# Kernel optimization log

Hardware: AMD Instinct MI355X
Metric: run time of the kernel (lower is better)

Reference implementation:

```python
import jax, jax.numpy as jnp
import numpy as np

# LIF decay constants: alpha = exp(-dt/tau_syn), beta = exp(-dt/tau_mem)
ALPHA = float(np.exp(-0.001 / 0.01))   # ~0.9048
BETA = float(np.exp(-0.001 / 0.005))   # ~0.8187


@jax.custom_vjp
def spike_fn(x):
    # HeavisideSigmoidApprox: Heaviside forward, sigmoid-derivative surrogate backward
    return (x > 0).astype(x.dtype)

def _spike_fwd(x):
    return spike_fn(x), x

def _spike_bwd(x, g):
    s = jax.nn.sigmoid(x)
    return (g * s * (1.0 - s),)

spike_fn.defvjp(_spike_fwd, _spike_bwd)


def lif_layer(spikes_in, W, R):
    """spikes_in: [B,T,F] -> (spikes [B,T,H], potentials [B,T,H])"""
    h = jnp.einsum('btf,fo->bto', spikes_in, W)  # [B,T,H]
    B, T, H = h.shape
    zeros = jnp.zeros((B, H), h.dtype)

    def step(carry, h_t):
        cur, pot, spk = carry
        rec = spk @ R                      # recurrent current from previous spikes
        new_spk = spike_fn(pot - 1.0)      # threshold at 1.0
        active = 1.0 - jax.lax.stop_gradient(new_spk)  # reset: .detach() in torch
        new_cur = ALPHA * cur + h_t + rec
        new_pot = (BETA * pot + new_cur) * active
        return (new_cur, new_pot, new_spk), (new_pot, new_spk)

    _, (pots, spks) = jax.lax.scan(step, (zeros, zeros, zeros), jnp.swapaxes(h, 0, 1))
    return jnp.swapaxes(spks, 0, 1), jnp.swapaxes(pots, 0, 1)


def readout_rnn(spikes, Wout):
    """spikes: [B,T,H] -> output potentials [B,T+1,O] (leading zero record)"""
    h = jnp.einsum('btf,fo->bto', spikes, Wout)  # [B,T,O]
    B, T, O = h.shape
    zeros = jnp.zeros((B, O), h.dtype)

    def step(carry, h_t):
        cur, pot = carry
        cur = ALPHA * cur + h_t
        pot = BETA * pot + cur
        return (cur, pot), pot

    _, pots = jax.lax.scan(step, (zeros, zeros), jnp.swapaxes(h, 0, 1))
    return jnp.concatenate([zeros[:, None, :], jnp.swapaxes(pots, 0, 1)], axis=1)


def _xavier(key, shape):
    std = np.sqrt(2.0 / (shape[0] + shape[1]))
    return jax.random.normal(key, shape, dtype=jnp.float32) * std


def setup_inputs() -> dict:
    key = jax.random.key(0)
    ks = jax.random.split(key, 6)
    B, T, F, H, O = 256, 100, 256, 1024, 8
    return {
        'inputs': jax.random.normal(ks[0], (B, T, F), dtype=jnp.float32),
        'W0': _xavier(ks[1], (F, H)),
        'W1': _xavier(ks[2], (H, H)),
        'R0': _xavier(ks[3], (H, H)),
        'R1': _xavier(ks[4], (H, H)),
        'Wout': _xavier(ks[5], (H, O)),
    }


def reference(inputs, W0, W1, R0, R1, Wout):
    s1, v1 = lif_layer(inputs, W0, R0)
    s2, v2 = lif_layer(s1, W1, R1)
    out = readout_rnn(s2, Wout)  # [B, T+1, O]
    return (out, s1, s2, v1, v2)
```

## Files before the change

### kernel.cpp

```cpp
#include <hip/hip_runtime.h>


#define SNN_B 256
#define SNN_T 100
#define SNN_F 256
#define SNN_H 1024
#define SNN_O 8

#define ALPHA 0.9048374180359595f
#define BETA  0.8187307530779818f

__global__ __launch_bounds__(256) void gemm_f32(
    const float* __restrict__ A, const float* __restrict__ Bm,
    float* __restrict__ C, int M, int N, int K)
{
    __shared__ float As[2][8][132];
    __shared__ float Bs[2][8][132];

    const int tid = threadIdx.x;
    const int m0 = blockIdx.y * 128;
    const int n0 = blockIdx.x * 128;
    const int ty = tid >> 4;
    const int tx = tid & 15;

    const int arow = tid >> 1;
    const int akq  = (tid & 1) * 4;
    const int bkr  = tid >> 5;
    const int bnq  = (tid & 31) * 4;

    const float* Aptr = A + (size_t)(m0 + arow) * K + akq;
    const float* Bptr = Bm + (size_t)bkr * N + n0 + bnq;

    float4 ar = *(const float4*)Aptr;
    float4 br = *(const float4*)Bptr;
    As[0][akq + 0][arow] = ar.x;
    As[0][akq + 1][arow] = ar.y;
    As[0][akq + 2][arow] = ar.z;
    As[0][akq + 3][arow] = ar.w;
    *(float4*)&Bs[0][bkr][bnq] = br;
    __syncthreads();

    float acc[8][8] = {};
    const int NK = K >> 3;

    for (int kt = 0; kt < NK; ++kt) {
        const int cur = kt & 1;
        if (kt + 1 < NK) {
            ar = *(const float4*)(Aptr + (kt + 1) * 8);
            br = *(const float4*)(Bptr + (size_t)(kt + 1) * 8 * N);
        }
        #pragma unroll
        for (int k = 0; k < 8; ++k) {
            const float4 a0 = *(const float4*)&As[cur][k][ty * 8];
            const float4 a1 = *(const float4*)&As[cur][k][ty * 8 + 4];
            const float4 b0 = *(const float4*)&Bs[cur][k][tx * 8];
            const float4 b1 = *(const float4*)&Bs[cur][k][tx * 8 + 4];
            const float am[8] = {a0.x, a0.y, a0.z, a0.w, a1.x, a1.y, a1.z, a1.w};
            const float bn[8] = {b0.x, b0.y, b0.z, b0.w, b1.x, b1.y, b1.z, b1.w};
            #pragma unroll
            for (int i = 0; i < 8; ++i)
                #pragma unroll
                for (int j = 0; j < 8; ++j)
                    acc[i][j] = fmaf(am[i], bn[j], acc[i][j]);
        }
        if (kt + 1 < NK) {
            const int nxt = cur ^ 1;
            __syncthreads();
            As[nxt][akq + 0][arow] = ar.x;
            As[nxt][akq + 1][arow] = ar.y;
            As[nxt][akq + 2][arow] = ar.z;
            As[nxt][akq + 3][arow] = ar.w;
            *(float4*)&Bs[nxt][bkr][bnq] = br;
            __syncthreads();
        }
    }

    #pragma unroll
    for (int i = 0; i < 8; ++i) {
        float* crow = C + (size_t)(m0 + ty * 8 + i) * N + n0 + tx * 8;
        *(float4*)crow = make_float4(acc[i][0], acc[i][1], acc[i][2], acc[i][3]);
        *(float4*)(crow + 4) = make_float4(acc[i][4], acc[i][5], acc[i][6], acc[i][7]);
    }
}


#define LIF_LOAD(Xa, Xb, Xc, Xd, Xe, Xf, Xg, Xh, cidx)                        \
    {                                                                         \
        const int4 ka_ = *(const int4*)&slist[(cidx) << 3];                   \
        const int4 kb_ = *(const int4*)&slist[(((cidx) << 3) + 4)];           \
        Xa = R[((unsigned)ka_.x << 10) | ctid];                               \
        Xb = R[((unsigned)ka_.y << 10) | ctid];                               \
        Xc = R[((unsigned)ka_.z << 10) | ctid];                               \
        Xd = R[((unsigned)ka_.w << 10) | ctid];                               \
        Xe = R[((unsigned)kb_.x << 10) | ctid];                               \
        Xf = R[((unsigned)kb_.y << 10) | ctid];                               \
        Xg = R[((unsigned)kb_.z << 10) | ctid];                               \
        Xh = R[((unsigned)kb_.w << 10) | ctid];                               \
    }

#define LIF_SUM(Xa, Xb, Xc, Xd, Xe, Xf, Xg, Xh)                               \
    {                                                                         \
        a0 += Xa; a0 += Xb; a0 += Xc; a0 += Xd;                               \
        a0 += Xe; a0 += Xf; a0 += Xg; a0 += Xh;                               \
    }

__global__ __launch_bounds__(1024) void lif_scan(
    const float* __restrict__ hbuf,
    const float* __restrict__ R,
    float* __restrict__ s_out,
    float* __restrict__ v_out)
{
    __shared__ __align__(16) int slist[SNN_H];
    __shared__ int wtot[16];
    __shared__ int sn;

    const int tid = threadIdx.x;
    const unsigned ctid = (unsigned)tid;
    const int b = blockIdx.x;
    const int wv = tid >> 6;
    const int lane = tid & 63;

    float cur = 0.f, pot = 0.f;

    if (tid == 0) sn = 0;
    __syncthreads();

    const float* hrow = hbuf + (size_t)b * SNN_T * SNN_H + tid;
    float*       srow = s_out + (size_t)b * SNN_T * SNN_H + tid;
    float*       vrow = v_out + (size_t)b * SNN_T * SNN_H + tid;

    for (int t = 0; t < SNN_T; ++t) {
        const float hv = *hrow;
        hrow += SNN_H;

        const int n = sn;
        float a0 = 0.f;
        int i = 0;
        const int nc = n >> 3;
        if (nc > 0) {
            float A0, A1, A2, A3, A4, A5, A6, A7;
            float B0, B1, B2, B3, B4, B5, B6, B7;
            LIF_LOAD(A0, A1, A2, A3, A4, A5, A6, A7, 0);
            int c = 1;
            for (; c + 1 < nc; c += 2) {
                LIF_LOAD(B0, B1, B2, B3, B4, B5, B6, B7, c);
                LIF_SUM(A0, A1, A2, A3, A4, A5, A6, A7);
                LIF_LOAD(A0, A1, A2, A3, A4, A5, A6, A7, c + 1);
                LIF_SUM(B0, B1, B2, B3, B4, B5, B6, B7);
            }
            if (c < nc) {
                LIF_LOAD(B0, B1, B2, B3, B4, B5, B6, B7, c);
                LIF_SUM(A0, A1, A2, A3, A4, A5, A6, A7);
                LIF_SUM(B0, B1, B2, B3, B4, B5, B6, B7);
            } else {
                LIF_SUM(A0, A1, A2, A3, A4, A5, A6, A7);
            }
            i = nc << 3;
        }
        for (; i < n; ++i)
            a0 += R[((unsigned)slist[i] << 10) | ctid];

        const bool p = (pot - 1.0f) > 0.0f;
        const float s = p ? 1.0f : 0.0f;
        cur = fmaf(ALPHA, cur, hv) + a0;
        pot = fmaf(BETA, pot, cur) * (1.0f - s);

        *srow = s;
        *vrow = pot;
        srow += SNN_H; vrow += SNN_H;

        const unsigned long long m = __ballot(p);
        const unsigned long long lt = (1ull << lane) - 1ull;
        const int lpre = __popcll(m & lt);
        if (lane == 0) wtot[wv] = __popcll(m);
        __syncthreads();
        int off = lpre;
        #pragma unroll
        for (int q = 0; q < 15; ++q)
            if (q < wv) off += wtot[q];
        if (p) slist[off] = tid;
        if (tid == 0) {
            int stot = 0;
            #pragma unroll
            for (int q = 0; q < 16; ++q) stot += wtot[q];
            sn = stot;
        }
        __syncthreads();
    }
}

__global__ __launch_bounds__(256) void readout_gemm(
    const float* __restrict__ s2in, const float* __restrict__ Wout,
    float* __restrict__ h3)
{
    const int gid = blockIdx.x * 256 + threadIdx.x;
    const int row = gid >> 3;
    const int o = gid & 7;
    const float* srow = s2in + (size_t)row * SNN_H;
    float acc = 0.f;
    for (int k = 0; k < SNN_H; k += 4) {
        float4 s = *(const float4*)&srow[k];
        acc = fmaf(s.x, Wout[(k + 0) * SNN_O + o], acc);
        acc = fmaf(s.y, Wout[(k + 1) * SNN_O + o], acc);
        acc = fmaf(s.z, Wout[(k + 2) * SNN_O + o], acc);
        acc = fmaf(s.w, Wout[(k + 3) * SNN_O + o], acc);
    }
    h3[(size_t)row * SNN_O + o] = acc;
}

__global__ __launch_bounds__(256) void readout_scan(
    const float* __restrict__ h3, float* __restrict__ out)
{
    const int gid = blockIdx.x * 256 + threadIdx.x;
    const int b = gid >> 3;
    const int o = gid & 7;
    float c = 0.f, p = 0.f;
    out[((size_t)b * (SNN_T + 1) + 0) * SNN_O + o] = 0.f;
    for (int t = 0; t < SNN_T; ++t) {
        c = fmaf(ALPHA, c, h3[((size_t)b * SNN_T + t) * SNN_O + o]);
        p = fmaf(BETA, p, c);
        out[((size_t)b * (SNN_T + 1) + t + 1) * SNN_O + o] = p;
    }
}

extern "C" void kernel_launch(void* const* d_in, const int* in_sizes, int n_in,
                              void* d_out, int out_size, void* d_ws, size_t ws_size,
                              hipStream_t stream)
{
    const float* X    = (const float*)d_in[0];
    const float* W0   = (const float*)d_in[1];
    const float* W1   = (const float*)d_in[2];
    const float* R0   = (const float*)d_in[3];
    const float* R1   = (const float*)d_in[4];
    const float* Wout = (const float*)d_in[5];

    const size_t BT_H = (size_t)SNN_B * SNN_T * SNN_H;
    float* out = (float*)d_out;
    float* s1  = out + (size_t)SNN_B * (SNN_T + 1) * SNN_O;
    float* s2  = s1 + BT_H;
    float* v1  = s2 + BT_H;
    float* v2  = v1 + BT_H;

    float* ws   = (float*)d_ws;
    float* hbuf = ws;
    float* h3   = hbuf + BT_H;

    const int M = SNN_B * SNN_T;

    gemm_f32<<<dim3(SNN_H / 128, M / 128), 256, 0, stream>>>(X, W0, hbuf, M, SNN_H, SNN_F);

    lif_scan<<<SNN_B, 1024, 0, stream>>>(hbuf, R0, s1, v1);

    gemm_f32<<<dim3(SNN_H / 128, M / 128), 256, 0, stream>>>(s1, W1, hbuf, M, SNN_H, SNN_H);

    lif_scan<<<SNN_B, 1024, 0, stream>>>(hbuf, R1, s2, v2);

    readout_gemm<<<(M * SNN_O) / 256, 256, 0, stream>>>(s2, Wout, h3);
    readout_scan<<<(SNN_B * SNN_O) / 256, 256, 0, stream>>>(h3, out);
}
```

Before: 3.108 ms.

## Deepen GEMM K-tile, pre-shift spike indices, restructure readout GEMM per row

The main GEMM now stages 16 K values per shared-memory tile instead of 8, which halves the number of barrier pairs per tile loop at the cost of more shared memory. The LIF scan stores spike indices already shifted to byte offsets, so each recurrent gather becomes a single OR plus byte-pointer load with no shift. The readout GEMM now has one thread per row that computes all 8 outputs, reading each spike row once instead of eight times and writing float4 results. The trade-off is fewer threads in the readout kernel.

New measurement: 3.393 ms. +9.2%, slower.

```diff
diff --git a/kernel.cpp b/kernel.cpp
--- a/kernel.cpp
+++ b/kernel.cpp
@@ -14,8 +14,8 @@
     const float* __restrict__ A, const float* __restrict__ Bm,
     float* __restrict__ C, int M, int N, int K)
 {
-    __shared__ float As[2][8][132];
-    __shared__ float Bs[2][8][132];
+    __shared__ float As[2][16][132];
+    __shared__ float Bs[2][16][132];
 
     const int tid = threadIdx.x;
     const int m0 = blockIdx.y * 128;
@@ -24,39 +24,50 @@
     const int tx = tid & 15;
 
     const int arow = tid >> 1;
-    const int akq  = (tid & 1) * 4;
-    const int bkr  = tid >> 5;
+    const int ak0  = (tid & 1) * 4;
+    const int bk0  = tid >> 5;
     const int bnq  = (tid & 31) * 4;
 
-    const float* Aptr = A + (size_t)(m0 + arow) * K + akq;
-    const float* Bptr = Bm + (size_t)bkr * N + n0 + bnq;
-
-    float4 ar = *(const float4*)Aptr;
-    float4 br = *(const float4*)Bptr;
-    As[0][akq + 0][arow] = ar.x;
-    As[0][akq + 1][arow] = ar.y;
-    As[0][akq + 2][arow] = ar.z;
-    As[0][akq + 3][arow] = ar.w;
-    *(float4*)&Bs[0][bkr][bnq] = br;
+    const float* Aptr = A + (size_t)(m0 + arow) * K;
+    const float* Bptr = Bm + n0 + bnq;
+
+    float4 a0r = *(const float4*)(Aptr + ak0);
+    float4 a1r = *(const float4*)(Aptr + ak0 + 8);
+    float4 b0r = *(const float4*)(Bptr + (size_t)bk0 * N);
+    float4 b1r = *(const float4*)(Bptr + (size_t)(bk0 + 8) * N);
+    As[0][ak0 + 0][arow] = a0r.x;
+    As[0][ak0 + 1][arow] = a0r.y;
+    As[0][ak0 + 2][arow] = a0r.z;
+    As[0][ak0 + 3][arow] = a0r.w;
+    As[0][ak0 + 8][arow] = a1r.x;
+    As[0][ak0 + 9][arow] = a1r.y;
+    As[0][ak0 + 10][arow] = a1r.z;
+    As[0][ak0 + 11][arow] = a1r.w;
+    *(float4*)&Bs[0][bk0][bnq] = b0r;
+    *(float4*)&Bs[0][bk0 + 8][bnq] = b1r;
     __syncthreads();
 
     float acc[8][8] = {};
-    const int NK = K >> 3;
+    const int NK = K >> 4;
 
     for (int kt = 0; kt < NK; ++kt) {
         const int cur = kt & 1;
         if (kt + 1 < NK) {
-            ar = *(const float4*)(Aptr + (kt + 1) * 8);
-            br = *(const float4*)(Bptr + (size_t)(kt + 1) * 8 * N);
+            const float* Ap = Aptr + (kt + 1) * 16;
+            const float* Bp = Bptr + (size_t)(kt + 1) * 16 * N;
+            a0r = *(const float4*)(Ap + ak0);
+            a1r = *(const float4*)(Ap + ak0 + 8);
+            b0r = *(const float4*)(Bp + (size_t)bk0 * N);
+            b1r = *(const float4*)(Bp + (size_t)(bk0 + 8) * N);
         }
         #pragma unroll
-        for (int k = 0; k < 8; ++k) {
-            const float4 a0 = *(const float4*)&As[cur][k][ty * 8];
-            const float4 a1 = *(const float4*)&As[cur][k][ty * 8 + 4];
-            const float4 b0 = *(const float4*)&Bs[cur][k][tx * 8];
-            const float4 b1 = *(const float4*)&Bs[cur][k][tx * 8 + 4];
-            const float am[8] = {a0.x, a0.y, a0.z, a0.w, a1.x, a1.y, a1.z, a1.w};
-            const float bn[8] = {b0.x, b0.y, b0.z, b0.w, b1.x, b1.y, b1.z, b1.w};
+        for (int k = 0; k < 16; ++k) {
+            const float4 av0 = *(const float4*)&As[cur][k][ty * 8];
+            const float4 av1 = *(const float4*)&As[cur][k][ty * 8 + 4];
+            const float4 bv0 = *(const float4*)&Bs[cur][k][tx * 8];
+            const float4 bv1 = *(const float4*)&Bs[cur][k][tx * 8 + 4];
+            const float am[8] = {av0.x, av0.y, av0.z, av0.w, av1.x, av1.y, av1.z, av1.w};
+            const float bn[8] = {bv0.x, bv0.y, bv0.z, bv0.w, bv1.x, bv1.y, bv1.z, bv1.w};
             #pragma unroll
             for (int i = 0; i < 8; ++i)
                 #pragma unroll
@@ -66,11 +77,16 @@
         if (kt + 1 < NK) {
             const int nxt = cur ^ 1;
             __syncthreads();
-            As[nxt][akq + 0][arow] = ar.x;
-            As[nxt][akq + 1][arow] = ar.y;
-            As[nxt][akq + 2][arow] = ar.z;
-            As[nxt][akq + 3][arow] = ar.w;
-            *(float4*)&Bs[nxt][bkr][bnq] = br;
+            As[nxt][ak0 + 0][arow] = a0r.x;
+            As[nxt][ak0 + 1][arow] = a0r.y;
+            As[nxt][ak0 + 2][arow] = a0r.z;
+            As[nxt][ak0 + 3][arow] = a0r.w;
+            As[nxt][ak0 + 8][arow] = a1r.x;
+            As[nxt][ak0 + 9][arow] = a1r.y;
+            As[nxt][ak0 + 10][arow] = a1r.z;
+            As[nxt][ak0 + 11][arow] = a1r.w;
+            *(float4*)&Bs[nxt][bk0][bnq] = b0r;
+            *(float4*)&Bs[nxt][bk0 + 8][bnq] = b1r;
             __syncthreads();
         }
     }
@@ -88,14 +104,14 @@
     {                                                                         \
         const int4 ka_ = *(const int4*)&slist[(cidx) << 3];                   \
         const int4 kb_ = *(const int4*)&slist[(((cidx) << 3) + 4)];           \
-        Xa = R[((unsigned)ka_.x << 10) | ctid];                               \
-        Xb = R[((unsigned)ka_.y << 10) | ctid];                               \
-        Xc = R[((unsigned)ka_.z << 10) | ctid];                               \
-        Xd = R[((unsigned)ka_.w << 10) | ctid];                               \
-        Xe = R[((unsigned)kb_.x << 10) | ctid];                               \
-        Xf = R[((unsigned)kb_.y << 10) | ctid];                               \
-        Xg = R[((unsigned)kb_.z << 10) | ctid];                               \
-        Xh = R[((unsigned)kb_.w << 10) | ctid];                               \
+        Xa = *(const float*)(Rb + (unsigned)(ka_.x | tid4));                  \
+        Xb = *(const float*)(Rb + (unsigned)(ka_.y | tid4));                  \
+        Xc = *(const float*)(Rb + (unsigned)(ka_.z | tid4));                  \
+        Xd = *(const float*)(Rb + (unsigned)(ka_.w | tid4));                  \
+        Xe = *(const float*)(Rb + (unsigned)(kb_.x | tid4));                  \
+        Xf = *(const float*)(Rb + (unsigned)(kb_.y | tid4));                  \
+        Xg = *(const float*)(Rb + (unsigned)(kb_.z | tid4));                  \
+        Xh = *(const float*)(Rb + (unsigned)(kb_.w | tid4));                  \
     }
 
 #define LIF_SUM(Xa, Xb, Xc, Xd, Xe, Xf, Xg, Xh)                               \
@@ -115,10 +131,11 @@
     __shared__ int sn;
 
     const int tid = threadIdx.x;
-    const unsigned ctid = (unsigned)tid;
+    const int tid4 = tid << 2;
     const int b = blockIdx.x;
     const int wv = tid >> 6;
     const int lane = tid & 63;
+    const char* __restrict__ Rb = (const char*)R;
 
     float cur = 0.f, pot = 0.f;
 
@@ -158,7 +175,7 @@
             i = nc << 3;
         }
         for (; i < n; ++i)
-            a0 += R[((unsigned)slist[i] << 10) | ctid];
+            a0 += *(const float*)(Rb + (unsigned)(slist[i] | tid4));
 
         const bool p = (pot - 1.0f) > 0.0f;
         const float s = p ? 1.0f : 0.0f;
@@ -178,7 +195,7 @@
         #pragma unroll
         for (int q = 0; q < 15; ++q)
             if (q < wv) off += wtot[q];
-        if (p) slist[off] = tid;
+        if (p) slist[off] = tid << 12;
         if (tid == 0) {
             int stot = 0;
             #pragma unroll
@@ -193,19 +210,21 @@
     const float* __restrict__ s2in, const float* __restrict__ Wout,
     float* __restrict__ h3)
 {
-    const int gid = blockIdx.x * 256 + threadIdx.x;
-    const int row = gid >> 3;
-    const int o = gid & 7;
+    const int row = blockIdx.x * 256 + threadIdx.x;
     const float* srow = s2in + (size_t)row * SNN_H;
-    float acc = 0.f;
+    float acc[8] = {};
     for (int k = 0; k < SNN_H; k += 4) {
-        float4 s = *(const float4*)&srow[k];
-        acc = fmaf(s.x, Wout[(k + 0) * SNN_O + o], acc);
-        acc = fmaf(s.y, Wout[(k + 1) * SNN_O + o], acc);
-        acc = fmaf(s.z, Wout[(k + 2) * SNN_O + o], acc);
-        acc = fmaf(s.w, Wout[(k + 3) * SNN_O + o], acc);
-    }
-    h3[(size_t)row * SNN_O + o] = acc;
+        const float4 s = *(const float4*)&srow[k];
+        const float sv[4] = {s.x, s.y, s.z, s.w};
+        #pragma unroll
+        for (int kk = 0; kk < 4; ++kk)
+            #pragma unroll
+            for (int o = 0; o < 8; ++o)
+                acc[o] = fmaf(sv[kk], Wout[(size_t)(k + kk) * SNN_O + o], acc[o]);
+    }
+    float* hp = h3 + (size_t)row * SNN_O;
+    *(float4*)hp = make_float4(acc[0], acc[1], acc[2], acc[3]);
+    *(float4*)(hp + 4) = make_float4(acc[4], acc[5], acc[6], acc[7]);
 }
 
 __global__ __launch_bounds__(256) void readout_scan(
@@ -255,6 +274,6 @@
 
     lif_scan<<<SNN_B, 1024, 0, stream>>>(hbuf, R1, s2, v2);
 
-    readout_gemm<<<(M * SNN_O) / 256, 256, 0, stream>>>(s2, Wout, h3);
+    readout_gemm<<<M / 256, 256, 0, stream>>>(s2, Wout, h3);
     readout_scan<<<(SNN_B * SNN_O) / 256, 256, 0, stream>>>(h3, out);
 }
```
